# Kernel tuning notes

Hardware: AMD Instinct MI355X
Metric: run time of the kernel (lower is better)

## Reference

```python
import jax, jax.numpy as jnp
import numpy as np

B, S, D, H = 2, 2048, 1024, 16
HD = D // H


def setup_inputs() -> dict:
    key = jax.random.key(0)
    ks = jax.random.split(key, 9)
    x = jax.random.normal(ks[0], (B, S, D), dtype=jnp.float32)
    scale = 1.0 / np.sqrt(D)
    Wq = jax.random.normal(ks[1], (D, D), dtype=jnp.float32) * scale
    bq = jnp.zeros((D,), dtype=jnp.float32)
    Wk = jax.random.normal(ks[2], (D, D), dtype=jnp.float32) * scale
    bk = jnp.zeros((D,), dtype=jnp.float32)
    Wv = jax.random.normal(ks[3], (D, D), dtype=jnp.float32) * scale
    bv = jnp.zeros((D,), dtype=jnp.float32)
    Wo = jax.random.normal(ks[4], (D, D), dtype=jnp.float32) * scale
    bo = jnp.zeros((D,), dtype=jnp.float32)
    return {"x": x, "Wq": Wq, "bq": bq, "Wk": Wk, "bk": bk,
            "Wv": Wv, "bv": bv, "Wo": Wo, "bo": bo}


def reference(x, Wq, bq, Wk, bk, Wv, bv, Wo, bo):
    b, s, d = x.shape
    h, hd = H, HD
    # torch Linear: y = x @ W.T + b
    q = (x @ Wq.T + bq).reshape(b, s, h, hd).transpose(0, 2, 1, 3)  # (b,h,s,hd)
    k = (x @ Wk.T + bk).reshape(b, s, h, hd).transpose(0, 2, 1, 3)
    v = (x @ Wv.T + bv).reshape(b, s, h, hd).transpose(0, 2, 1, 3)
    scores = jnp.einsum('bhqd,bhkd->bhqk', q, k) / np.sqrt(hd)  # (b,h,s,s)
    # FAITHFUL to source: softmax over dim=1 (head axis), not the key axis.
    attn = jax.nn.softmax(scores, axis=1)
    # dropout is identity at inference
    out = jnp.einsum('bhqk,bhkd->bhqd', attn, v)  # (b,h,s,hd)
    out = out.transpose(0, 2, 1, 3).reshape(b, s, d)
    return out @ Wo.T + bo
```

## Files before the change

kernel.cpp:

```cpp
#include <hip/hip_runtime.h>
#include <hip/hip_bf16.h>
#include <cstdint>
#include <cstddef>


typedef __bf16 bf16x8 __attribute__((ext_vector_type(8)));
typedef __bf16 bf16x4 __attribute__((ext_vector_type(4)));
typedef _Float16 f16x4 __attribute__((ext_vector_type(4)));
typedef _Float16 f16x8 __attribute__((ext_vector_type(8)));
typedef float floatx4 __attribute__((ext_vector_type(4)));

#define S_LEN 2048
#define DIM 1024
#define NH 16
#define HD 64
#define MTOT 4096
#define C_EXP 0.1803368801111244f

__device__ __forceinline__ float fast_exp2(float x) { return __builtin_amdgcn_exp2f(x); }

__device__ __forceinline__ void g2l16(const void* g, void* l) {
    __builtin_amdgcn_global_load_lds(
        (const __attribute__((address_space(1))) void*)g,
        (__attribute__((address_space(3))) void*)l, 16, 0, 0);
}

__global__ void cast_f32_bf16(const float* __restrict__ s, __bf16* __restrict__ d, int n) {
    int i = (blockIdx.x * blockDim.x + threadIdx.x) * 4;
    if (i < n) {
        float4 v = *(const float4*)&s[i];
        bf16x4 o;
        o.x = (__bf16)v.x; o.y = (__bf16)v.y; o.z = (__bf16)v.z; o.w = (__bf16)v.w;
        *(bf16x4*)&d[i] = o;
    }
}

__global__ void cast_w4(const float* __restrict__ w0, const float* __restrict__ w1,
                        const float* __restrict__ w2, const float* __restrict__ w3,
                        __bf16* __restrict__ o0, __bf16* __restrict__ o1,
                        __bf16* __restrict__ o2, _Float16* __restrict__ o3, int n) {
    int i = (blockIdx.x * blockDim.x + threadIdx.x) * 4;
    if (i >= n) return;
    if (blockIdx.y == 3) {
        float4 v = *(const float4*)&w3[i];
        f16x4 o;
        o[0] = (_Float16)v.x; o[1] = (_Float16)v.y; o[2] = (_Float16)v.z; o[3] = (_Float16)v.w;
        *(f16x4*)&o3[i] = o;
        return;
    }
    const float* s; __bf16* d;
    switch (blockIdx.y) {
        case 0: s = w0; d = o0; break;
        case 1: s = w1; d = o1; break;
        default: s = w2; d = o2; break;
    }
    float4 v = *(const float4*)&s[i];
    bf16x4 o;
    o.x = (__bf16)v.x; o.y = (__bf16)v.y; o.z = (__bf16)v.z; o.w = (__bf16)v.w;
    *(bf16x4*)&d[i] = o;
}

__global__ __launch_bounds__(256, 2) void qkv_gemm(const __bf16* __restrict__ A,
                                                   const __bf16* __restrict__ Wq,
                                                   const __bf16* __restrict__ Wk,
                                                   const __bf16* __restrict__ Wv,
                                                   const float* __restrict__ bq,
                                                   const float* __restrict__ bk,
                                                   const float* __restrict__ bv,
                                                   __bf16* __restrict__ Qo,
                                                   __bf16* __restrict__ Ko,
                                                   _Float16* __restrict__ Vt) {
    const int tng = blockIdx.x * 128, tm = blockIdx.y * 128;
    const int wsel = tng >> 10, tn = tng & 1023;
    const __bf16* W = (wsel == 0) ? Wq : (wsel == 1) ? Wk : Wv;
    const float* bias = (wsel == 0) ? bq : (wsel == 1) ? bk : bv;
    __shared__ __bf16 As[128 * 32];
    __shared__ __bf16 Bs[128 * 32];
    const int tid = threadIdx.x, wid = tid >> 6, lane = tid & 63;
    const int l15 = lane & 15, quad = lane >> 4;
    const int wm = (wid >> 1) * 64, wn = (wid & 1) * 64;
    floatx4 acc[4][4] = {};
    for (int k0 = 0; k0 < DIM; k0 += 32) {
        __syncthreads();
#pragma unroll
        for (int i = 0; i < 2; ++i) {
            int slot = i * 256 + tid;
            int r = slot >> 2, c8 = (slot & 3) * 8;
            g2l16(&A[(size_t)(tm + r) * DIM + k0 + c8], &As[slot * 8]);
            g2l16(&W[(size_t)(tn + r) * DIM + k0 + c8], &Bs[slot * 8]);
        }
        __syncthreads();
        bf16x8 af[4], bf[4];
#pragma unroll
        for (int t = 0; t < 4; ++t) {
            af[t] = *(const bf16x8*)&As[(wm + t * 16 + l15) * 32 + quad * 8];
            bf[t] = *(const bf16x8*)&Bs[(wn + t * 16 + l15) * 32 + quad * 8];
        }
#pragma unroll
        for (int im = 0; im < 4; ++im)
#pragma unroll
            for (int in = 0; in < 4; ++in)
                acc[im][in] = __builtin_amdgcn_mfma_f32_16x16x32_bf16(af[im], bf[in], acc[im][in], 0, 0, 0);
    }
    if (wsel < 2) {
        __bf16* O = wsel ? Ko : Qo;
#pragma unroll
        for (int im = 0; im < 4; ++im)
#pragma unroll
            for (int in = 0; in < 4; ++in)
#pragma unroll
                for (int r = 0; r < 4; ++r) {
                    int row = tm + wm + im * 16 + quad * 4 + r;
                    int col = tn + wn + in * 16 + l15;
                    O[(size_t)row * DIM + col] = (__bf16)(acc[im][in][r] + bias[col]);
                }
    } else {
#pragma unroll
        for (int im = 0; im < 4; ++im)
#pragma unroll
            for (int in = 0; in < 4; ++in) {
                int cv = tn + wn + in * 16 + l15;
                int row4 = tm + wm + im * 16 + quad * 4;
                float bv_ = bias[cv];
                f16x4 o;
#pragma unroll
                for (int r = 0; r < 4; ++r) o[r] = (_Float16)(acc[im][in][r] + bv_);
                *(f16x4*)&Vt[(size_t)cv * MTOT + row4] = o;
            }
    }
}

__global__ __launch_bounds__(256, 8) void den4(const __bf16* __restrict__ Q,
                                               const __bf16* __restrict__ Km,
                                               __bf16* __restrict__ rd) {
    const int kt = blockIdx.x * 64, qt = blockIdx.y * 64, b = blockIdx.z;
    __shared__ __bf16 Ks[2 * 2 * 64 * 32];
    const int tid = threadIdx.x, wid = tid >> 6, lane = tid & 63;
    const int l15 = lane & 15, quad = lane >> 4;
    const int wq = wid * 16;
    floatx4 dsum[4] = {};
    const size_t qrow = (size_t)(b * S_LEN + qt + wq + l15) * DIM;
    for (int hh = 0; hh < 8; ++hh) {
        __syncthreads();
#pragma unroll
        for (int i = 0; i < 4; ++i) {
            int slot = i * 256 + tid;
            int hs = slot >> 9, rem = slot & 511;
            int p = rem >> 8, rem2 = rem & 255;
            int r = rem2 >> 2, c8 = (rem2 & 3) * 8;
            g2l16(&Km[(size_t)(b * S_LEN + kt + r) * DIM + (hh * 2 + hs) * HD + p * 32 + c8],
                  &Ks[slot * 8]);
        }
        __syncthreads();
#pragma unroll
        for (int hs = 0; hs < 2; ++hs) {
            int h = hh * 2 + hs;
            bf16x8 af0 = *(const bf16x8*)&Q[qrow + h * HD + quad * 8];
            bf16x8 af1 = *(const bf16x8*)&Q[qrow + h * HD + 32 + quad * 8];
#pragma unroll
            for (int n = 0; n < 4; ++n) {
                bf16x8 b0 = *(const bf16x8*)&Ks[hs * 4096 + (n * 16 + l15) * 32 + quad * 8];
                bf16x8 b1 = *(const bf16x8*)&Ks[hs * 4096 + 2048 + (n * 16 + l15) * 32 + quad * 8];
                floatx4 acc = {};
                acc = __builtin_amdgcn_mfma_f32_16x16x32_bf16(af0, b0, acc, 0, 0, 0);
                acc = __builtin_amdgcn_mfma_f32_16x16x32_bf16(af1, b1, acc, 0, 0, 0);
#pragma unroll
                for (int r = 0; r < 4; ++r) dsum[n][r] += fast_exp2(acc[r] * C_EXP);
            }
        }
    }
#pragma unroll
    for (int n = 0; n < 4; ++n)
#pragma unroll
        for (int r = 0; r < 4; ++r) {
            int q = qt + wq + quad * 4 + r;
            int k = kt + n * 16 + l15;
            rd[(size_t)(b * S_LEN + q) * S_LEN + k] = (__bf16)(1.0f / dsum[n][r]);
        }
}

__global__ __launch_bounds__(256, 8) void attn4(const __bf16* __restrict__ Q,
                                                const __bf16* __restrict__ Km,
                                                const _Float16* __restrict__ Vt,
                                                const __bf16* __restrict__ rd,
                                                _Float16* __restrict__ AO1,
                                                _Float16* __restrict__ AO2) {
    const int qt = (blockIdx.x >> 1) * 64, ks = blockIdx.x & 1;
    const int h = blockIdx.y, b = blockIdx.z;
    __shared__ __bf16 Ks[2 * 64 * 32];
    __shared__ _Float16 Vts[64 * 72];
    const int tid = threadIdx.x, wid = tid >> 6, lane = tid & 63;
    const int l15 = lane & 15, quad = lane >> 4;
    const int wq = wid * 16;
    const size_t qrow = (size_t)(b * S_LEN + qt + wq + l15) * DIM + h * HD;
    bf16x8 qf0 = *(const bf16x8*)&Q[qrow + quad * 8];
    bf16x8 qf1 = *(const bf16x8*)&Q[qrow + 32 + quad * 8];
    const __bf16* rdrow = &rd[(size_t)(b * S_LEN + qt + wq + l15) * S_LEN];
    floatx4 oacc[4] = {};
    const int kt0 = ks * (S_LEN / 2), kt1 = kt0 + S_LEN / 2;
    for (int kt = kt0; kt < kt1; kt += 64) {
        __syncthreads();
#pragma unroll
        for (int i = 0; i < 2; ++i) {
            int slot = i * 256 + tid;
            int p = slot >> 8, rem = slot & 255;
            int r = rem >> 2, c8 = (rem & 3) * 8;
            g2l16(&Km[(size_t)(b * S_LEN + kt + r) * DIM + h * HD + p * 32 + c8], &Ks[slot * 8]);
        }
#pragma unroll
        for (int i = 0; i < 2; ++i) {
            int slot = i * 256 + tid;
            int r = slot >> 3, c = (slot & 7) * 8;
            *(f16x8*)&Vts[r * 72 + c] =
                *(const f16x8*)&Vt[(size_t)(h * HD + r) * MTOT + b * S_LEN + kt + c];
        }
        __syncthreads();
#pragma unroll
        for (int mp = 0; mp < 4; ++mp) {
            bf16x8 kf0 = *(const bf16x8*)&Ks[(mp * 16 + l15) * 32 + quad * 8];
            bf16x8 kf1 = *(const bf16x8*)&Ks[2048 + (mp * 16 + l15) * 32 + quad * 8];
            floatx4 s = {};
            s = __builtin_amdgcn_mfma_f32_16x16x32_bf16(kf0, qf0, s, 0, 0, 0);
            s = __builtin_amdgcn_mfma_f32_16x16x32_bf16(kf1, qf1, s, 0, 0, 0);
            bf16x4 rv = *(const bf16x4*)&rdrow[kt + mp * 16 + quad * 4];
            f16x4 pa;
#pragma unroll
            for (int r = 0; r < 4; ++r)
                pa[r] = (_Float16)(fast_exp2(s[r] * C_EXP) * (float)rv[r]);
#pragma unroll
            for (int n = 0; n < 4; ++n) {
                f16x4 vb = *(const f16x4*)&Vts[(n * 16 + l15) * 72 + mp * 16 + quad * 4];
                oacc[n] = __builtin_amdgcn_mfma_f32_16x16x16f16(pa, vb, oacc[n], 0, 0, 0);
            }
        }
    }
    _Float16* AO = ks ? AO2 : AO1;
#pragma unroll
    for (int n = 0; n < 4; ++n)
#pragma unroll
        for (int r = 0; r < 4; ++r) {
            int row = qt + wq + quad * 4 + r;
            int col = h * HD + n * 16 + l15;
            AO[(size_t)(b * S_LEN + row) * DIM + col] = (_Float16)oacc[n][r];
        }
}

__global__ __launch_bounds__(256, 2) void gemm_out2(const _Float16* __restrict__ A1,
                                                    const _Float16* __restrict__ A2,
                                                    const _Float16* __restrict__ Bw,
                                                    const float* __restrict__ bias,
                                                    float* __restrict__ C) {
    const int tm = blockIdx.y * 128, tn = blockIdx.x * 64;
    __shared__ _Float16 As1[2 * 128 * 32];
    __shared__ _Float16 As2[2 * 128 * 32];
    __shared__ _Float16 Bs[2 * 64 * 32];
    const int tid = threadIdx.x, wid = tid >> 6, lane = tid & 63;
    const int l15 = lane & 15, quad = lane >> 4;
    const int wm = (wid >> 1) * 64, wn = (wid & 1) * 32;
    floatx4 acc[4][2] = {};
    for (int k0 = 0; k0 < DIM; k0 += 64) {
        __syncthreads();
#pragma unroll
        for (int i = 0; i < 4; ++i) {
            int slot = i * 256 + tid;
            int p = slot >> 9, rem = slot & 511;
            int r = rem >> 2, c8 = (rem & 3) * 8;
            size_t ga = (size_t)(tm + r) * DIM + k0 + p * 32 + c8;
            g2l16(&A1[ga], &As1[slot * 8]);
            g2l16(&A2[ga], &As2[slot * 8]);
        }
#pragma unroll
        for (int i = 0; i < 2; ++i) {
            int slot = i * 256 + tid;
            int p = slot >> 8, rem = slot & 255;
            int r = rem >> 2, c8 = (rem & 3) * 8;
            g2l16(&Bw[(size_t)(tn + r) * DIM + k0 + p * 32 + c8], &Bs[slot * 8]);
        }
        __syncthreads();
#pragma unroll
        for (int kc = 0; kc < 2; ++kc) {
            f16x8 af[4], bf[2];
#pragma unroll
            for (int t = 0; t < 4; ++t) {
                int off = kc * 4096 + (wm + t * 16 + l15) * 32 + quad * 8;
                f16x8 a1 = *(const f16x8*)&As1[off];
                f16x8 a2 = *(const f16x8*)&As2[off];
                af[t] = a1 + a2;
            }
#pragma unroll
            for (int t = 0; t < 2; ++t)
                bf[t] = *(const f16x8*)&Bs[kc * 2048 + (wn + t * 16 + l15) * 32 + quad * 8];
#pragma unroll
            for (int im = 0; im < 4; ++im)
#pragma unroll
                for (int in = 0; in < 2; ++in)
                    acc[im][in] = __builtin_amdgcn_mfma_f32_16x16x32_f16(af[im], bf[in], acc[im][in], 0, 0, 0);
        }
    }
#pragma unroll
    for (int im = 0; im < 4; ++im)
#pragma unroll
        for (int in = 0; in < 2; ++in)
#pragma unroll
            for (int r = 0; r < 4; ++r) {
                int row = tm + wm + im * 16 + quad * 4 + r;
                int col = tn + wn + in * 16 + l15;
                C[(size_t)row * DIM + col] = acc[im][in][r] + bias[col];
            }
}

extern "C" void kernel_launch(void* const* d_in, const int* in_sizes, int n_in,
                              void* d_out, int out_size, void* d_ws, size_t ws_size,
                              hipStream_t stream) {
    const float* x  = (const float*)d_in[0];
    const float* Wq = (const float*)d_in[1];
    const float* bq = (const float*)d_in[2];
    const float* Wk = (const float*)d_in[3];
    const float* bk = (const float*)d_in[4];
    const float* Wv = (const float*)d_in[5];
    const float* bv = (const float*)d_in[6];
    const float* Wo = (const float*)d_in[7];
    const float* bo = (const float*)d_in[8];
    float* out = (float*)d_out;

    char* ws = (char*)d_ws;
    const size_t MB = 1u << 20;
    __bf16*    xb  = (__bf16*)(ws);
    __bf16*    Wqb = (__bf16*)(ws + 8 * MB);
    __bf16*    Wkb = (__bf16*)(ws + 10 * MB);
    __bf16*    Wvb = (__bf16*)(ws + 12 * MB);
    _Float16*  Wof = (_Float16*)(ws + 14 * MB);
    __bf16*    Qb  = (__bf16*)(ws + 16 * MB);
    __bf16*    Kb  = (__bf16*)(ws + 24 * MB);
    _Float16*  VtH = (_Float16*)(ws + 32 * MB);
    __bf16*    rd  = (__bf16*)(ws + 40 * MB);
    _Float16*  AO1 = (_Float16*)(ws + 56 * MB);
    _Float16*  AO2 = (_Float16*)(ws + 64 * MB);

    cast_f32_bf16<<<4096, 256, 0, stream>>>(x, xb, MTOT * DIM);
    cast_w4<<<dim3(1024, 4), 256, 0, stream>>>(Wq, Wk, Wv, Wo, Wqb, Wkb, Wvb, Wof, DIM * DIM);

    qkv_gemm<<<dim3(24, 32), 256, 0, stream>>>(xb, Wqb, Wkb, Wvb, bq, bk, bv, Qb, Kb, VtH);

    den4<<<dim3(S_LEN / 64, S_LEN / 64, 2), 256, 0, stream>>>(Qb, Kb, rd);

    attn4<<<dim3((S_LEN / 64) * 2, NH, 2), 256, 0, stream>>>(Qb, Kb, VtH, rd, AO1, AO2);

    gemm_out2<<<dim3(DIM / 64, MTOT / 128), 256, 0, stream>>>(AO1, AO2, Wof, bo, out);
}
```

Before: 289.3 us.

## Double-buffer K/V tiles in den and attn kernels, widen attn query tile

Both attention-stage kernels now double-buffer their shared-memory K (and V) tiles, issuing the next tile's loads before computing on the current one. This removes one barrier per iteration and lets global-load latency overlap with MFMA and exp work. The attention kernel also gives each wave 32 query rows instead of 16, so every K/V tile loaded into LDS is reused across twice as many queries and the grid is halved. In exchange, shared memory and register use roughly double and the launch-bounds occupancy hint drops from 8 to 4 blocks.

Measured after the change: 277.5 us. 1.04x faster.

```diff
diff --git a/kernel.cpp b/kernel.cpp
--- a/kernel.cpp
+++ b/kernel.cpp
@@ -130,40 +130,55 @@
     }
 }
 
-__global__ __launch_bounds__(256, 8) void den4(const __bf16* __restrict__ Q,
+__global__ __launch_bounds__(256, 4) void den6(const __bf16* __restrict__ Q,
                                                const __bf16* __restrict__ Km,
                                                __bf16* __restrict__ rd) {
     const int kt = blockIdx.x * 64, qt = blockIdx.y * 64, b = blockIdx.z;
-    __shared__ __bf16 Ks[2 * 2 * 64 * 32];
+    __shared__ __bf16 Ks[2][2 * 2 * 64 * 32];
     const int tid = threadIdx.x, wid = tid >> 6, lane = tid & 63;
     const int l15 = lane & 15, quad = lane >> 4;
     const int wq = wid * 16;
     floatx4 dsum[4] = {};
     const size_t qrow = (size_t)(b * S_LEN + qt + wq + l15) * DIM;
+    const size_t kbase = (size_t)(b * S_LEN + kt) * DIM;
+
+#pragma unroll
+    for (int i = 0; i < 4; ++i) {
+        int slot = i * 256 + tid;
+        int hs = slot >> 9, rem = slot & 511;
+        int p = rem >> 8, rem2 = rem & 255;
+        int r = rem2 >> 2, c8 = (rem2 & 3) * 8;
+        g2l16(&Km[kbase + (size_t)r * DIM + hs * HD + p * 32 + c8], &Ks[0][slot * 8]);
+    }
     for (int hh = 0; hh < 8; ++hh) {
-        __syncthreads();
-#pragma unroll
-        for (int i = 0; i < 4; ++i) {
-            int slot = i * 256 + tid;
-            int hs = slot >> 9, rem = slot & 511;
-            int p = rem >> 8, rem2 = rem & 255;
-            int r = rem2 >> 2, c8 = (rem2 & 3) * 8;
-            g2l16(&Km[(size_t)(b * S_LEN + kt + r) * DIM + (hh * 2 + hs) * HD + p * 32 + c8],
-                  &Ks[slot * 8]);
-        }
-        __syncthreads();
+        const int cur = hh & 1, nxt = cur ^ 1;
+        __syncthreads();
+        bf16x8 af[2][2];
 #pragma unroll
         for (int hs = 0; hs < 2; ++hs) {
-            int h = hh * 2 + hs;
-            bf16x8 af0 = *(const bf16x8*)&Q[qrow + h * HD + quad * 8];
-            bf16x8 af1 = *(const bf16x8*)&Q[qrow + h * HD + 32 + quad * 8];
+            af[hs][0] = *(const bf16x8*)&Q[qrow + (hh * 2 + hs) * HD + quad * 8];
+            af[hs][1] = *(const bf16x8*)&Q[qrow + (hh * 2 + hs) * HD + 32 + quad * 8];
+        }
+        if (hh + 1 < 8) {
+#pragma unroll
+            for (int i = 0; i < 4; ++i) {
+                int slot = i * 256 + tid;
+                int hs = slot >> 9, rem = slot & 511;
+                int p = rem >> 8, rem2 = rem & 255;
+                int r = rem2 >> 2, c8 = (rem2 & 3) * 8;
+                g2l16(&Km[kbase + (size_t)r * DIM + ((hh + 1) * 2 + hs) * HD + p * 32 + c8],
+                      &Ks[nxt][slot * 8]);
+            }
+        }
+#pragma unroll
+        for (int hs = 0; hs < 2; ++hs) {
 #pragma unroll
             for (int n = 0; n < 4; ++n) {
-                bf16x8 b0 = *(const bf16x8*)&Ks[hs * 4096 + (n * 16 + l15) * 32 + quad * 8];
-                bf16x8 b1 = *(const bf16x8*)&Ks[hs * 4096 + 2048 + (n * 16 + l15) * 32 + quad * 8];
+                bf16x8 b0 = *(const bf16x8*)&Ks[cur][hs * 4096 + (n * 16 + l15) * 32 + quad * 8];
+                bf16x8 b1 = *(const bf16x8*)&Ks[cur][hs * 4096 + 2048 + (n * 16 + l15) * 32 + quad * 8];
                 floatx4 acc = {};
-                acc = __builtin_amdgcn_mfma_f32_16x16x32_bf16(af0, b0, acc, 0, 0, 0);
-                acc = __builtin_amdgcn_mfma_f32_16x16x32_bf16(af1, b1, acc, 0, 0, 0);
+                acc = __builtin_amdgcn_mfma_f32_16x16x32_bf16(af[hs][0], b0, acc, 0, 0, 0);
+                acc = __builtin_amdgcn_mfma_f32_16x16x32_bf16(af[hs][1], b1, acc, 0, 0, 0);
 #pragma unroll
                 for (int r = 0; r < 4; ++r) dsum[n][r] += fast_exp2(acc[r] * C_EXP);
             }
@@ -179,70 +194,121 @@
         }
 }
 
-__global__ __launch_bounds__(256, 8) void attn4(const __bf16* __restrict__ Q,
+__global__ __launch_bounds__(256, 4) void attn6(const __bf16* __restrict__ Q,
                                                 const __bf16* __restrict__ Km,
                                                 const _Float16* __restrict__ Vt,
                                                 const __bf16* __restrict__ rd,
                                                 _Float16* __restrict__ AO1,
                                                 _Float16* __restrict__ AO2) {
-    const int qt = (blockIdx.x >> 1) * 64, ks = blockIdx.x & 1;
+    const int qt = (blockIdx.x >> 1) * 128, ks = blockIdx.x & 1;
     const int h = blockIdx.y, b = blockIdx.z;
-    __shared__ __bf16 Ks[2 * 64 * 32];
-    __shared__ _Float16 Vts[64 * 72];
+    __shared__ __bf16 Ks[2][2 * 64 * 32];
+    __shared__ _Float16 Vts[2][64 * 72];
     const int tid = threadIdx.x, wid = tid >> 6, lane = tid & 63;
     const int l15 = lane & 15, quad = lane >> 4;
-    const int wq = wid * 16;
-    const size_t qrow = (size_t)(b * S_LEN + qt + wq + l15) * DIM + h * HD;
-    bf16x8 qf0 = *(const bf16x8*)&Q[qrow + quad * 8];
-    bf16x8 qf1 = *(const bf16x8*)&Q[qrow + 32 + quad * 8];
-    const __bf16* rdrow = &rd[(size_t)(b * S_LEN + qt + wq + l15) * S_LEN];
-    floatx4 oacc[4] = {};
-    const int kt0 = ks * (S_LEN / 2), kt1 = kt0 + S_LEN / 2;
-    for (int kt = kt0; kt < kt1; kt += 64) {
-        __syncthreads();
+    const int wq = wid * 32;
+    const size_t qrow0 = (size_t)(b * S_LEN + qt + wq + l15) * DIM + h * HD;
+    const size_t qrow1 = qrow0 + 16 * DIM;
+    bf16x8 qf[2][2];
+    qf[0][0] = *(const bf16x8*)&Q[qrow0 + quad * 8];
+    qf[0][1] = *(const bf16x8*)&Q[qrow0 + 32 + quad * 8];
+    qf[1][0] = *(const bf16x8*)&Q[qrow1 + quad * 8];
+    qf[1][1] = *(const bf16x8*)&Q[qrow1 + 32 + quad * 8];
+    const __bf16* rdrow0 = &rd[(size_t)(b * S_LEN + qt + wq + l15) * S_LEN];
+    const __bf16* rdrow1 = rdrow0 + (size_t)16 * S_LEN;
+    floatx4 oacc[2][4] = {};
+    const int kt0 = ks * (S_LEN / 2);
+    const size_t kdim = (size_t)b * S_LEN * DIM;
+
+    {
+        f16x8 vtmp[2];
+#pragma unroll
+        for (int i = 0; i < 2; ++i) {
+            int slot = i * 256 + tid;
+            int r = slot >> 3, c = (slot & 7) * 8;
+            vtmp[i] = *(const f16x8*)&Vt[(size_t)(h * HD + r) * MTOT + b * S_LEN + kt0 + c];
+        }
 #pragma unroll
         for (int i = 0; i < 2; ++i) {
             int slot = i * 256 + tid;
             int p = slot >> 8, rem = slot & 255;
             int r = rem >> 2, c8 = (rem & 3) * 8;
-            g2l16(&Km[(size_t)(b * S_LEN + kt + r) * DIM + h * HD + p * 32 + c8], &Ks[slot * 8]);
+            g2l16(&Km[kdim + (size_t)(kt0 + r) * DIM + h * HD + p * 32 + c8], &Ks[0][slot * 8]);
         }
 #pragma unroll
         for (int i = 0; i < 2; ++i) {
             int slot = i * 256 + tid;
             int r = slot >> 3, c = (slot & 7) * 8;
-            *(f16x8*)&Vts[r * 72 + c] =
-                *(const f16x8*)&Vt[(size_t)(h * HD + r) * MTOT + b * S_LEN + kt + c];
-        }
-        __syncthreads();
+            *(f16x8*)&Vts[0][r * 72 + c] = vtmp[i];
+        }
+    }
+    for (int it = 0; it < 16; ++it) {
+        const int cur = it & 1, nxt = cur ^ 1;
+        const int kt = kt0 + it * 64;
+        __syncthreads();
+        bf16x4 rv[2][4];
 #pragma unroll
         for (int mp = 0; mp < 4; ++mp) {
-            bf16x8 kf0 = *(const bf16x8*)&Ks[(mp * 16 + l15) * 32 + quad * 8];
-            bf16x8 kf1 = *(const bf16x8*)&Ks[2048 + (mp * 16 + l15) * 32 + quad * 8];
-            floatx4 s = {};
-            s = __builtin_amdgcn_mfma_f32_16x16x32_bf16(kf0, qf0, s, 0, 0, 0);
-            s = __builtin_amdgcn_mfma_f32_16x16x32_bf16(kf1, qf1, s, 0, 0, 0);
-            bf16x4 rv = *(const bf16x4*)&rdrow[kt + mp * 16 + quad * 4];
-            f16x4 pa;
-#pragma unroll
-            for (int r = 0; r < 4; ++r)
-                pa[r] = (_Float16)(fast_exp2(s[r] * C_EXP) * (float)rv[r]);
+            rv[0][mp] = *(const bf16x4*)&rdrow0[kt + mp * 16 + quad * 4];
+            rv[1][mp] = *(const bf16x4*)&rdrow1[kt + mp * 16 + quad * 4];
+        }
+        if (it + 1 < 16) {
+            const int ktn = kt + 64;
+            f16x8 vtmp[2];
+#pragma unroll
+            for (int i = 0; i < 2; ++i) {
+                int slot = i * 256 + tid;
+                int r = slot >> 3, c = (slot & 7) * 8;
+                vtmp[i] = *(const f16x8*)&Vt[(size_t)(h * HD + r) * MTOT + b * S_LEN + ktn + c];
+            }
+#pragma unroll
+            for (int i = 0; i < 2; ++i) {
+                int slot = i * 256 + tid;
+                int p = slot >> 8, rem = slot & 255;
+                int r = rem >> 2, c8 = (rem & 3) * 8;
+                g2l16(&Km[kdim + (size_t)(ktn + r) * DIM + h * HD + p * 32 + c8], &Ks[nxt][slot * 8]);
+            }
+#pragma unroll
+            for (int i = 0; i < 2; ++i) {
+                int slot = i * 256 + tid;
+                int r = slot >> 3, c = (slot & 7) * 8;
+                *(f16x8*)&Vts[nxt][r * 72 + c] = vtmp[i];
+            }
+        }
+#pragma unroll
+        for (int mp = 0; mp < 4; ++mp) {
+            bf16x8 kf0 = *(const bf16x8*)&Ks[cur][(mp * 16 + l15) * 32 + quad * 8];
+            bf16x8 kf1 = *(const bf16x8*)&Ks[cur][2048 + (mp * 16 + l15) * 32 + quad * 8];
+            floatx4 s0 = {}, s1 = {};
+            s0 = __builtin_amdgcn_mfma_f32_16x16x32_bf16(kf0, qf[0][0], s0, 0, 0, 0);
+            s0 = __builtin_amdgcn_mfma_f32_16x16x32_bf16(kf1, qf[0][1], s0, 0, 0, 0);
+            s1 = __builtin_amdgcn_mfma_f32_16x16x32_bf16(kf0, qf[1][0], s1, 0, 0, 0);
+            s1 = __builtin_amdgcn_mfma_f32_16x16x32_bf16(kf1, qf[1][1], s1, 0, 0, 0);
+            f16x4 pa0, pa1;
+#pragma unroll
+            for (int r = 0; r < 4; ++r) {
+                pa0[r] = (_Float16)(fast_exp2(s0[r] * C_EXP) * (float)rv[0][mp][r]);
+                pa1[r] = (_Float16)(fast_exp2(s1[r] * C_EXP) * (float)rv[1][mp][r]);
+            }
 #pragma unroll
             for (int n = 0; n < 4; ++n) {
-                f16x4 vb = *(const f16x4*)&Vts[(n * 16 + l15) * 72 + mp * 16 + quad * 4];
-                oacc[n] = __builtin_amdgcn_mfma_f32_16x16x16f16(pa, vb, oacc[n], 0, 0, 0);
+                f16x4 vb = *(const f16x4*)&Vts[cur][(n * 16 + l15) * 72 + mp * 16 + quad * 4];
+                oacc[0][n] = __builtin_amdgcn_mfma_f32_16x16x16f16(pa0, vb, oacc[0][n], 0, 0, 0);
+                oacc[1][n] = __builtin_amdgcn_mfma_f32_16x16x16f16(pa1, vb, oacc[1][n], 0, 0, 0);
             }
         }
     }
     _Float16* AO = ks ? AO2 : AO1;
 #pragma unroll
-    for (int n = 0; n < 4; ++n)
-#pragma unroll
-        for (int r = 0; r < 4; ++r) {
-            int row = qt + wq + quad * 4 + r;
-            int col = h * HD + n * 16 + l15;
-            AO[(size_t)(b * S_LEN + row) * DIM + col] = (_Float16)oacc[n][r];
-        }
+    for (int np = 0; np < 2; ++np)
+#pragma unroll
+        for (int n = 0; n < 4; ++n)
+#pragma unroll
+            for (int r = 0; r < 4; ++r) {
+                int row = qt + wq + np * 16 + quad * 4 + r;
+                int col = h * HD + n * 16 + l15;
+                AO[(size_t)(b * S_LEN + row) * DIM + col] = (_Float16)oacc[np][n][r];
+            }
 }
 
 __global__ __launch_bounds__(256, 2) void gemm_out2(const _Float16* __restrict__ A1,
@@ -342,9 +408,9 @@
 
     qkv_gemm<<<dim3(24, 32), 256, 0, stream>>>(xb, Wqb, Wkb, Wvb, bq, bk, bv, Qb, Kb, VtH);
 
-    den4<<<dim3(S_LEN / 64, S_LEN / 64, 2), 256, 0, stream>>>(Qb, Kb, rd);
-
-    attn4<<<dim3((S_LEN / 64) * 2, NH, 2), 256, 0, stream>>>(Qb, Kb, VtH, rd, AO1, AO2);
+    den6<<<dim3(S_LEN / 64, S_LEN / 64, 2), 256, 0, stream>>>(Qb, Kb, rd);
+
+    attn6<<<dim3((S_LEN / 128) * 2, NH, 2), 256, 0, stream>>>(Qb, Kb, VtH, rd, AO1, AO2);
 
     gemm_out2<<<dim3(DIM / 64, MTOT / 128), 256, 0, stream>>>(AO1, AO2, Wof, bo, out);
 }
```

## Double-buffer K/V tiles in den and attn kernels, widen blocks, merge casts

Applied to the files above, without the earlier changes.

The denominator and attention kernels now use 512-thread blocks covering 128 query rows, so each K/V tile loaded into LDS is shared by twice as many warps. Both kernels double-buffer their LDS tiles, prefetching the next head or key tile while MFMAs run on the current one, and drop one barrier per iteration. The separate x and weight cast kernels are merged into one launch. This costs twice the LDS per block and may lower occupancy; the prefetch reuses the single remaining barrier for ordering.

After: 272.6 us. 5.8% less time.

```diff
diff --git a/kernel.cpp b/kernel.cpp
--- a/kernel.cpp
+++ b/kernel.cpp
@@ -25,35 +25,33 @@
         (__attribute__((address_space(3))) void*)l, 16, 0, 0);
 }
 
-__global__ void cast_f32_bf16(const float* __restrict__ s, __bf16* __restrict__ d, int n) {
-    int i = (blockIdx.x * blockDim.x + threadIdx.x) * 4;
-    if (i < n) {
-        float4 v = *(const float4*)&s[i];
+__global__ void cast_all(const float* __restrict__ x,
+                         const float* __restrict__ w0, const float* __restrict__ w1,
+                         const float* __restrict__ w2, const float* __restrict__ w3,
+                         __bf16* __restrict__ xb,
+                         __bf16* __restrict__ o0, __bf16* __restrict__ o1,
+                         __bf16* __restrict__ o2, _Float16* __restrict__ o3) {
+    int bid = blockIdx.x;
+    if (bid < 4096) {
+        int i = (bid * 256 + threadIdx.x) * 4;
+        float4 v = *(const float4*)&x[i];
         bf16x4 o;
         o.x = (__bf16)v.x; o.y = (__bf16)v.y; o.z = (__bf16)v.z; o.w = (__bf16)v.w;
-        *(bf16x4*)&d[i] = o;
-    }
-}
-
-__global__ void cast_w4(const float* __restrict__ w0, const float* __restrict__ w1,
-                        const float* __restrict__ w2, const float* __restrict__ w3,
-                        __bf16* __restrict__ o0, __bf16* __restrict__ o1,
-                        __bf16* __restrict__ o2, _Float16* __restrict__ o3, int n) {
-    int i = (blockIdx.x * blockDim.x + threadIdx.x) * 4;
-    if (i >= n) return;
-    if (blockIdx.y == 3) {
+        *(bf16x4*)&xb[i] = o;
+        return;
+    }
+    bid -= 4096;
+    int wi = bid >> 10;
+    int i = ((bid & 1023) * 256 + threadIdx.x) * 4;
+    if (wi == 3) {
         float4 v = *(const float4*)&w3[i];
         f16x4 o;
         o[0] = (_Float16)v.x; o[1] = (_Float16)v.y; o[2] = (_Float16)v.z; o[3] = (_Float16)v.w;
         *(f16x4*)&o3[i] = o;
         return;
     }
-    const float* s; __bf16* d;
-    switch (blockIdx.y) {
-        case 0: s = w0; d = o0; break;
-        case 1: s = w1; d = o1; break;
-        default: s = w2; d = o2; break;
-    }
+    const float* s = (wi == 0) ? w0 : (wi == 1) ? w1 : w2;
+    __bf16* d = (wi == 0) ? o0 : (wi == 1) ? o1 : o2;
     float4 v = *(const float4*)&s[i];
     bf16x4 o;
     o.x = (__bf16)v.x; o.y = (__bf16)v.y; o.z = (__bf16)v.z; o.w = (__bf16)v.w;
@@ -130,40 +128,55 @@
     }
 }
 
-__global__ __launch_bounds__(256, 8) void den4(const __bf16* __restrict__ Q,
+__global__ __launch_bounds__(512, 8) void den7(const __bf16* __restrict__ Q,
                                                const __bf16* __restrict__ Km,
                                                __bf16* __restrict__ rd) {
-    const int kt = blockIdx.x * 64, qt = blockIdx.y * 64, b = blockIdx.z;
-    __shared__ __bf16 Ks[2 * 2 * 64 * 32];
+    const int kt = blockIdx.x * 64, qt = blockIdx.y * 128, b = blockIdx.z;
+    __shared__ __bf16 Ks[2][2 * 2 * 64 * 32];
     const int tid = threadIdx.x, wid = tid >> 6, lane = tid & 63;
     const int l15 = lane & 15, quad = lane >> 4;
     const int wq = wid * 16;
     floatx4 dsum[4] = {};
     const size_t qrow = (size_t)(b * S_LEN + qt + wq + l15) * DIM;
+    const size_t kbase = (size_t)(b * S_LEN + kt) * DIM;
+
+#pragma unroll
+    for (int i = 0; i < 2; ++i) {
+        int slot = i * 512 + tid;
+        int hs = slot >> 9, rem = slot & 511;
+        int p = rem >> 8, rem2 = rem & 255;
+        int r = rem2 >> 2, c8 = (rem2 & 3) * 8;
+        g2l16(&Km[kbase + (size_t)r * DIM + hs * HD + p * 32 + c8], &Ks[0][slot * 8]);
+    }
     for (int hh = 0; hh < 8; ++hh) {
-        __syncthreads();
-#pragma unroll
-        for (int i = 0; i < 4; ++i) {
-            int slot = i * 256 + tid;
-            int hs = slot >> 9, rem = slot & 511;
-            int p = rem >> 8, rem2 = rem & 255;
-            int r = rem2 >> 2, c8 = (rem2 & 3) * 8;
-            g2l16(&Km[(size_t)(b * S_LEN + kt + r) * DIM + (hh * 2 + hs) * HD + p * 32 + c8],
-                  &Ks[slot * 8]);
-        }
-        __syncthreads();
+        const int cur = hh & 1, nxt = cur ^ 1;
+        __syncthreads();
+        bf16x8 af[2][2];
 #pragma unroll
         for (int hs = 0; hs < 2; ++hs) {
-            int h = hh * 2 + hs;
-            bf16x8 af0 = *(const bf16x8*)&Q[qrow + h * HD + quad * 8];
-            bf16x8 af1 = *(const bf16x8*)&Q[qrow + h * HD + 32 + quad * 8];
+            af[hs][0] = *(const bf16x8*)&Q[qrow + (hh * 2 + hs) * HD + quad * 8];
+            af[hs][1] = *(const bf16x8*)&Q[qrow + (hh * 2 + hs) * HD + 32 + quad * 8];
+        }
+        if (hh + 1 < 8) {
+#pragma unroll
+            for (int i = 0; i < 2; ++i) {
+                int slot = i * 512 + tid;
+                int hs = slot >> 9, rem = slot & 511;
+                int p = rem >> 8, rem2 = rem & 255;
+                int r = rem2 >> 2, c8 = (rem2 & 3) * 8;
+                g2l16(&Km[kbase + (size_t)r * DIM + ((hh + 1) * 2 + hs) * HD + p * 32 + c8],
+                      &Ks[nxt][slot * 8]);
+            }
+        }
+#pragma unroll
+        for (int hs = 0; hs < 2; ++hs) {
 #pragma unroll
             for (int n = 0; n < 4; ++n) {
-                bf16x8 b0 = *(const bf16x8*)&Ks[hs * 4096 + (n * 16 + l15) * 32 + quad * 8];
-                bf16x8 b1 = *(const bf16x8*)&Ks[hs * 4096 + 2048 + (n * 16 + l15) * 32 + quad * 8];
+                bf16x8 b0 = *(const bf16x8*)&Ks[cur][hs * 4096 + (n * 16 + l15) * 32 + quad * 8];
+                bf16x8 b1 = *(const bf16x8*)&Ks[cur][hs * 4096 + 2048 + (n * 16 + l15) * 32 + quad * 8];
                 floatx4 acc = {};
-                acc = __builtin_amdgcn_mfma_f32_16x16x32_bf16(af0, b0, acc, 0, 0, 0);
-                acc = __builtin_amdgcn_mfma_f32_16x16x32_bf16(af1, b1, acc, 0, 0, 0);
+                acc = __builtin_amdgcn_mfma_f32_16x16x32_bf16(af[hs][0], b0, acc, 0, 0, 0);
+                acc = __builtin_amdgcn_mfma_f32_16x16x32_bf16(af[hs][1], b1, acc, 0, 0, 0);
 #pragma unroll
                 for (int r = 0; r < 4; ++r) dsum[n][r] += fast_exp2(acc[r] * C_EXP);
             }
@@ -179,16 +192,16 @@
         }
 }
 
-__global__ __launch_bounds__(256, 8) void attn4(const __bf16* __restrict__ Q,
+__global__ __launch_bounds__(512, 8) void attn7(const __bf16* __restrict__ Q,
                                                 const __bf16* __restrict__ Km,
                                                 const _Float16* __restrict__ Vt,
                                                 const __bf16* __restrict__ rd,
                                                 _Float16* __restrict__ AO1,
                                                 _Float16* __restrict__ AO2) {
-    const int qt = (blockIdx.x >> 1) * 64, ks = blockIdx.x & 1;
+    const int qt = (blockIdx.x >> 1) * 128, ks = blockIdx.x & 1;
     const int h = blockIdx.y, b = blockIdx.z;
-    __shared__ __bf16 Ks[2 * 64 * 32];
-    __shared__ _Float16 Vts[64 * 72];
+    __shared__ __bf16 Ks[2][2 * 64 * 32];
+    __shared__ _Float16 Vts[2][64 * 72];
     const int tid = threadIdx.x, wid = tid >> 6, lane = tid & 63;
     const int l15 = lane & 15, quad = lane >> 4;
     const int wq = wid * 16;
@@ -197,28 +210,34 @@
     bf16x8 qf1 = *(const bf16x8*)&Q[qrow + 32 + quad * 8];
     const __bf16* rdrow = &rd[(size_t)(b * S_LEN + qt + wq + l15) * S_LEN];
     floatx4 oacc[4] = {};
-    const int kt0 = ks * (S_LEN / 2), kt1 = kt0 + S_LEN / 2;
-    for (int kt = kt0; kt < kt1; kt += 64) {
-        __syncthreads();
-#pragma unroll
-        for (int i = 0; i < 2; ++i) {
-            int slot = i * 256 + tid;
-            int p = slot >> 8, rem = slot & 255;
+    const int kt0 = ks * (S_LEN / 2);
+    const size_t kdim = (size_t)b * S_LEN * DIM;
+
+    {
+        int vr = tid >> 3, vc = (tid & 7) * 8;
+        f16x8 vtmp = *(const f16x8*)&Vt[(size_t)(h * HD + vr) * MTOT + b * S_LEN + kt0 + vc];
+        int p = tid >> 8, rem = tid & 255;
+        int r = rem >> 2, c8 = (rem & 3) * 8;
+        g2l16(&Km[kdim + (size_t)(kt0 + r) * DIM + h * HD + p * 32 + c8], &Ks[0][tid * 8]);
+        *(f16x8*)&Vts[0][vr * 72 + vc] = vtmp;
+    }
+    for (int it = 0; it < 16; ++it) {
+        const int cur = it & 1, nxt = cur ^ 1;
+        const int kt = kt0 + it * 64;
+        __syncthreads();
+        if (it + 1 < 16) {
+            const int ktn = kt + 64;
+            int vr = tid >> 3, vc = (tid & 7) * 8;
+            f16x8 vtmp = *(const f16x8*)&Vt[(size_t)(h * HD + vr) * MTOT + b * S_LEN + ktn + vc];
+            int p = tid >> 8, rem = tid & 255;
             int r = rem >> 2, c8 = (rem & 3) * 8;
-            g2l16(&Km[(size_t)(b * S_LEN + kt + r) * DIM + h * HD + p * 32 + c8], &Ks[slot * 8]);
-        }
-#pragma unroll
-        for (int i = 0; i < 2; ++i) {
-            int slot = i * 256 + tid;
-            int r = slot >> 3, c = (slot & 7) * 8;
-            *(f16x8*)&Vts[r * 72 + c] =
-                *(const f16x8*)&Vt[(size_t)(h * HD + r) * MTOT + b * S_LEN + kt + c];
-        }
-        __syncthreads();
+            g2l16(&Km[kdim + (size_t)(ktn + r) * DIM + h * HD + p * 32 + c8], &Ks[nxt][tid * 8]);
+            *(f16x8*)&Vts[nxt][vr * 72 + vc] = vtmp;
+        }
 #pragma unroll
         for (int mp = 0; mp < 4; ++mp) {
-            bf16x8 kf0 = *(const bf16x8*)&Ks[(mp * 16 + l15) * 32 + quad * 8];
-            bf16x8 kf1 = *(const bf16x8*)&Ks[2048 + (mp * 16 + l15) * 32 + quad * 8];
+            bf16x8 kf0 = *(const bf16x8*)&Ks[cur][(mp * 16 + l15) * 32 + quad * 8];
+            bf16x8 kf1 = *(const bf16x8*)&Ks[cur][2048 + (mp * 16 + l15) * 32 + quad * 8];
             floatx4 s = {};
             s = __builtin_amdgcn_mfma_f32_16x16x32_bf16(kf0, qf0, s, 0, 0, 0);
             s = __builtin_amdgcn_mfma_f32_16x16x32_bf16(kf1, qf1, s, 0, 0, 0);
@@ -229,7 +248,7 @@
                 pa[r] = (_Float16)(fast_exp2(s[r] * C_EXP) * (float)rv[r]);
 #pragma unroll
             for (int n = 0; n < 4; ++n) {
-                f16x4 vb = *(const f16x4*)&Vts[(n * 16 + l15) * 72 + mp * 16 + quad * 4];
+                f16x4 vb = *(const f16x4*)&Vts[cur][(n * 16 + l15) * 72 + mp * 16 + quad * 4];
                 oacc[n] = __builtin_amdgcn_mfma_f32_16x16x16f16(pa, vb, oacc[n], 0, 0, 0);
             }
         }
@@ -337,14 +356,13 @@
     _Float16*  AO1 = (_Float16*)(ws + 56 * MB);
     _Float16*  AO2 = (_Float16*)(ws + 64 * MB);
 
-    cast_f32_bf16<<<4096, 256, 0, stream>>>(x, xb, MTOT * DIM);
-    cast_w4<<<dim3(1024, 4), 256, 0, stream>>>(Wq, Wk, Wv, Wo, Wqb, Wkb, Wvb, Wof, DIM * DIM);
+    cast_all<<<8192, 256, 0, stream>>>(x, Wq, Wk, Wv, Wo, xb, Wqb, Wkb, Wvb, Wof);
 
     qkv_gemm<<<dim3(24, 32), 256, 0, stream>>>(xb, Wqb, Wkb, Wvb, bq, bk, bv, Qb, Kb, VtH);
 
-    den4<<<dim3(S_LEN / 64, S_LEN / 64, 2), 256, 0, stream>>>(Qb, Kb, rd);
-
-    attn4<<<dim3((S_LEN / 64) * 2, NH, 2), 256, 0, stream>>>(Qb, Kb, VtH, rd, AO1, AO2);
+    den7<<<dim3(S_LEN / 64, S_LEN / 128, 2), 512, 0, stream>>>(Qb, Kb, rd);
+
+    attn7<<<dim3((S_LEN / 128) * 2, NH, 2), 512, 0, stream>>>(Qb, Kb, VtH, rd, AO1, AO2);
 
     gemm_out2<<<dim3(DIM / 64, MTOT / 128), 256, 0, stream>>>(AO1, AO2, Wof, bo, out);
 }
```
